# Optimization experiments

Measured on AMD Instinct MI355X. Metric: run time of the kernel, lower is better.

## Reference

```python
import jax, jax.numpy as jnp
import numpy as np

D_MODEL = 1024
NUM_HEADS = 16
HEAD_DIM = D_MODEL // NUM_HEADS
B, T = 4, 2048


def setup_inputs() -> dict:
    key = jax.random.key(0)
    ks = jax.random.split(key, 6)
    s = 1.0 / np.sqrt(D_MODEL)  # ~ nn.Linear init scale
    return {
        "x_q": jax.random.normal(ks[0], (B, T, D_MODEL), jnp.float32),
        "x_kv": jax.random.normal(ks[1], (B, T, D_MODEL), jnp.float32),
        "Wq": jax.random.uniform(ks[2], (D_MODEL, D_MODEL), jnp.float32, -s, s),
        "Wk": jax.random.uniform(ks[3], (D_MODEL, D_MODEL), jnp.float32, -s, s),
        "Wv": jax.random.uniform(ks[4], (D_MODEL, D_MODEL), jnp.float32, -s, s),
        "Wo": jax.random.uniform(ks[5], (D_MODEL, D_MODEL), jnp.float32, -s, s),
    }


def reference(x_q, x_kv, Wq, Wk, Wv, Wo):
    Bq, Tq, C = x_q.shape
    Tk = x_kv.shape[1]
    # torch nn.Linear: y = x @ W.T
    q = (x_q @ Wq.T).reshape(Bq, Tq, NUM_HEADS, HEAD_DIM).transpose(0, 2, 1, 3)
    k = (x_kv @ Wk.T).reshape(Bq, Tk, NUM_HEADS, HEAD_DIM).transpose(0, 2, 1, 3)
    v = (x_kv @ Wv.T).reshape(Bq, Tk, NUM_HEADS, HEAD_DIM).transpose(0, 2, 1, 3)
    scores = jnp.einsum("bhqd,bhkd->bhqk", q, k) / jnp.sqrt(
        jnp.asarray(HEAD_DIM, x_q.dtype)
    )
    causal = jnp.triu(jnp.ones((Tq, Tk), bool), k=1)  # True above diagonal
    scores = jnp.where(causal, -jnp.inf, scores)
    attn = jax.nn.softmax(scores, axis=-1)
    out = jnp.einsum("bhqk,bhkd->bhqd", attn, v)
    out = out.transpose(0, 2, 1, 3).reshape(Bq, Tq, C)
    return out @ Wo.T
```

## Files before the change

kernel.cpp:

```cpp
#include <hip/hip_runtime.h>
#include <stdint.h>

#define T_SEQ 2048
#define NH 16
#define HD 64
#define DM 1024
#define BB 4
#define MROWS (BB * T_SEQ)

typedef __attribute__((ext_vector_type(8))) __bf16 bf16x8;
typedef __attribute__((ext_vector_type(8))) unsigned short u16x8;
typedef __attribute__((ext_vector_type(4))) unsigned short u16x4;
typedef __attribute__((ext_vector_type(4))) float f32x4;

__device__ __forceinline__ unsigned short f2bf(float f) {
  unsigned int x = __float_as_uint(f);
  x = (x + 0x7fffu + ((x >> 16) & 1u)) >> 16;
  return (unsigned short)x;
}

__device__ __forceinline__ bf16x8 ld8_f32(const float* __restrict__ p) {
  f32x4 a = *(const f32x4*)p;
  f32x4 b = *(const f32x4*)(p + 4);
  u16x8 u;
#pragma unroll
  for (int i = 0; i < 4; ++i) {
    u[i]     = f2bf(a[i]);
    u[i + 4] = f2bf(b[i]);
  }
  return __builtin_bit_cast(bf16x8, u);
}

__device__ __forceinline__ bf16x8 ld8_bf(const unsigned short* p) {
  return __builtin_bit_cast(bf16x8, *(const u16x8*)p);
}

__device__ __forceinline__ bf16x8 ld8_lds(const unsigned short* p) {
  u16x4 a = *(const u16x4*)p;
  u16x4 b = *(const u16x4*)(p + 4);
  return __builtin_bit_cast(bf16x8,
      __builtin_shufflevector(a, b, 0, 1, 2, 3, 4, 5, 6, 7));
}

__device__ __forceinline__ u16x4 lo4(u16x8 v) {
  return __builtin_shufflevector(v, v, 0, 1, 2, 3);
}
__device__ __forceinline__ u16x4 hi4(u16x8 v) {
  return __builtin_shufflevector(v, v, 4, 5, 6, 7);
}

__device__ __forceinline__ void gload_lds16(const unsigned short* g,
                                            unsigned short* l) {
  __builtin_amdgcn_global_load_lds(
      (const __attribute__((address_space(1))) unsigned int*)g,
      (__attribute__((address_space(3))) unsigned int*)l, 16, 0, 0);
}

__global__ __launch_bounds__(256) void conv_f32_bf16(
    const float* __restrict__ src, unsigned short* __restrict__ dst, int n8) {
  const int i = blockIdx.x * 256 + threadIdx.x;
  if (i < n8)
    *(u16x8*)(dst + (size_t)i * 8) =
        __builtin_bit_cast(u16x8, ld8_f32(src + (size_t)i * 8));
}

__global__ __launch_bounds__(256) void conv_w4(
    const float* __restrict__ s0, const float* __restrict__ s1,
    const float* __restrict__ s2, const float* __restrict__ s3,
    unsigned short* __restrict__ d012, unsigned short* __restrict__ d3,
    int n8) {
  const int y = blockIdx.y;
  const float* src = (y == 0) ? s0 : (y == 1) ? s1 : (y == 2) ? s2 : s3;
  unsigned short* dst = (y < 3) ? d012 + (size_t)y * DM * DM : d3;
  const int i = blockIdx.x * 256 + threadIdx.x;
  if (i < n8)
    *(u16x8*)(dst + (size_t)i * 8) =
        __builtin_bit_cast(u16x8, ld8_f32(src + (size_t)i * 8));
}

template <int MODE>
__global__ __launch_bounds__(256) void gemm128(
    const unsigned short* __restrict__ A, const unsigned short* __restrict__ B,
    void* __restrict__ Cv, int M, int N, int K) {
  __shared__ __align__(16) unsigned short As[2][128 * 32];
  __shared__ __align__(16) unsigned short Bs[2][128 * 32];

  const int t = threadIdx.x;
  const int lane = t & 63, wave = t >> 6;
  const int m0 = blockIdx.y * 128, n0 = blockIdx.x * 128;

  const int srow = t >> 2;
  const int scol = (t & 3) * 8;
  const unsigned short* ga0 = A + (size_t)(m0 + srow) * K + scol;
  const unsigned short* ga1 = A + (size_t)(m0 + 64 + srow) * K + scol;
  const unsigned short* gb0 = B + (size_t)(n0 + srow) * K + scol;
  const unsigned short* gb1 = B + (size_t)(n0 + 64 + srow) * K + scol;
  const int lo0 = (wave * 16) * 32, lo1 = (64 + wave * 16) * 32;

  const int mw = (wave >> 1) * 64, nw = (wave & 1) * 64;
  const int fr = lane & 15, fq = (lane >> 4) * 8;

  f32x4 acc[4][4];
#pragma unroll
  for (int i = 0; i < 4; ++i)
#pragma unroll
    for (int j = 0; j < 4; ++j) acc[i][j] = (f32x4){0.f, 0.f, 0.f, 0.f};

  for (int k0 = 0; k0 < K; k0 += 64) {
    __syncthreads();
    gload_lds16(ga0 + k0, &As[0][lo0]);
    gload_lds16(ga1 + k0, &As[0][lo1]);
    gload_lds16(gb0 + k0, &Bs[0][lo0]);
    gload_lds16(gb1 + k0, &Bs[0][lo1]);
    gload_lds16(ga0 + k0 + 32, &As[1][lo0]);
    gload_lds16(ga1 + k0 + 32, &As[1][lo1]);
    gload_lds16(gb0 + k0 + 32, &Bs[1][lo0]);
    gload_lds16(gb1 + k0 + 32, &Bs[1][lo1]);
    __syncthreads();

#pragma unroll
    for (int ks = 0; ks < 2; ++ks) {
      bf16x8 af[4], bfr[4];
#pragma unroll
      for (int i = 0; i < 4; ++i)
        af[i] = ld8_bf(&As[ks][(mw + i * 16 + fr) * 32 + fq]);
#pragma unroll
      for (int j = 0; j < 4; ++j)
        bfr[j] = ld8_bf(&Bs[ks][(nw + j * 16 + fr) * 32 + fq]);
#pragma unroll
      for (int i = 0; i < 4; ++i)
#pragma unroll
        for (int j = 0; j < 4; ++j)
          acc[i][j] = __builtin_amdgcn_mfma_f32_16x16x32_bf16(
              af[i], bfr[j], acc[i][j], 0, 0, 0);
    }
  }

  const int orow = (lane >> 4) * 4, ocol = lane & 15;
#pragma unroll
  for (int i = 0; i < 4; ++i)
#pragma unroll
    for (int j = 0; j < 4; ++j) {
      if constexpr (MODE == 2) {
        const int mb = m0 + mw + i * 16 + orow;
        const int n = n0 + nw + j * 16 + ocol;
        u16x4 pk;
#pragma unroll
        for (int r = 0; r < 4; ++r) pk[r] = f2bf(acc[i][j][r]);
        unsigned short* dst = (unsigned short*)Cv +
            ((size_t)((mb >> 11) * NH + (n >> 6)) * HD + (n & 63)) * T_SEQ +
            (mb & 2047);
        *(u16x4*)dst = pk;
      } else {
#pragma unroll
        for (int r = 0; r < 4; ++r) {
          const size_t idx = (size_t)(m0 + mw + i * 16 + orow + r) * N +
                             (n0 + nw + j * 16 + ocol);
          if constexpr (MODE == 1)
            ((float*)Cv)[idx] = acc[i][j][r];
          else
            ((unsigned short*)Cv)[idx] = f2bf(acc[i][j][r]);
        }
      }
    }
}

#define ASTR 68

__global__ __launch_bounds__(256, 2) void attn_flash2(
    const unsigned short* Qw, const unsigned short* __restrict__ Kw,
    const unsigned short* __restrict__ Vt, unsigned short* Ow) {
  __shared__ __align__(16) unsigned short k_lds[2][64][ASTR];
  __shared__ __align__(16) unsigned short vt_lds[2][64][ASTR];
  __shared__ __align__(16) unsigned short p_lds[4][32][ASTR];
  __shared__ float alpha_lds[4][32];
  __shared__ float l_lds[4][32];

  const int tid = threadIdx.x, lane = tid & 63, wave = tid >> 6;
  const int c16 = lane & 15, quad = lane >> 4;
  const int b = blockIdx.z, h = blockIdx.y;
  const int pi = blockIdx.x;
  const int qb0A = (15 - pi) * 128;
  const int qb0B = pi * 128;
  const size_t rkbase = (size_t)b * T_SEQ * DM + (size_t)h * HD;
  const size_t vtbase = (size_t)(b * NH + h) * HD * T_SEQ;

  const int q_loA = qb0A + wave * 32;
  const int q_loB = qb0B + wave * 32;

  bf16x8 qfA[2][2], qfB[2][2];
#pragma unroll
  for (int nf = 0; nf < 2; ++nf) {
    const unsigned short* qpA =
        Qw + rkbase + (size_t)(q_loA + nf * 16 + c16) * DM + quad * 8;
    qfA[nf][0] = ld8_bf(qpA);
    qfA[nf][1] = ld8_bf(qpA + 32);
    const unsigned short* qpB =
        Qw + rkbase + (size_t)(q_loB + nf * 16 + c16) * DM + quad * 8;
    qfB[nf][0] = ld8_bf(qpB);
    qfB[nf][1] = ld8_bf(qpB + 32);
  }

  f32x4 oA[2][4], oB[2][4];
#pragma unroll
  for (int nf = 0; nf < 2; ++nf)
#pragma unroll
    for (int j = 0; j < 4; ++j) {
      oA[nf][j] = (f32x4){0.f, 0.f, 0.f, 0.f};
      oB[nf][j] = (f32x4){0.f, 0.f, 0.f, 0.f};
    }
  float mA[2] = {-3.0e38f, -3.0e38f}, lA[2] = {0.f, 0.f};
  float mB[2] = {-3.0e38f, -3.0e38f}, lB[2] = {0.f, 0.f};

  const int srow = tid >> 2;
  const int scol = (tid & 3) * 16;
  const int ntiles = (qb0A + 191) >> 6;
  const int ntA_w = (q_loA + 95) >> 6;
  const int ntB_w = (q_loB + 95) >> 6;

  const unsigned short* kp0 = Kw + rkbase + (size_t)srow * DM + scol;
  const unsigned short* vp0 = Vt + vtbase + (size_t)srow * T_SEQ + scol;

  auto subtile = [&](const bf16x8 (&qf)[2][2], f32x4 (&o)[2][4],
                     float (&m_r)[2], float (&l_r)[2], const int q_lo,
                     const int kb0, const int bi) {
    f32x4 s[4][2];
    __builtin_amdgcn_s_setprio(1);
#pragma unroll
    for (int mf = 0; mf < 4; ++mf) {
      const unsigned short* kr = &k_lds[bi][mf * 16 + c16][quad * 8];
      const bf16x8 k0 = ld8_lds(kr);
      const bf16x8 k1 = ld8_lds(kr + 32);
#pragma unroll
      for (int nf = 0; nf < 2; ++nf) {
        f32x4 a = {0.f, 0.f, 0.f, 0.f};
        a = __builtin_amdgcn_mfma_f32_16x16x32_bf16(k0, qf[nf][0], a, 0, 0, 0);
        a = __builtin_amdgcn_mfma_f32_16x16x32_bf16(k1, qf[nf][1], a, 0, 0, 0);
        s[mf][nf] = a;
      }
    }
    __builtin_amdgcn_s_setprio(0);
    if (kb0 + 63 > q_lo) {
#pragma unroll
      for (int mf = 0; mf < 4; ++mf) {
        const int key0 = kb0 + mf * 16 + quad * 4;
#pragma unroll
        for (int nf = 0; nf < 2; ++nf) {
          const int qg = q_lo + nf * 16 + c16;
#pragma unroll
          for (int r = 0; r < 4; ++r)
            s[mf][nf][r] =
                (key0 + r <= qg) ? s[mf][nf][r] * 0.125f : -3.0e38f;
        }
      }
    } else {
#pragma unroll
      for (int mf = 0; mf < 4; ++mf)
#pragma unroll
        for (int nf = 0; nf < 2; ++nf)
#pragma unroll
          for (int r = 0; r < 4; ++r) s[mf][nf][r] *= 0.125f;
    }

#pragma unroll
    for (int nf = 0; nf < 2; ++nf) {
      float mx = -3.0e38f;
#pragma unroll
      for (int mf = 0; mf < 4; ++mf)
#pragma unroll
        for (int r = 0; r < 4; ++r) mx = fmaxf(mx, s[mf][nf][r]);
      mx = fmaxf(mx, __shfl_xor(mx, 16, 64));
      mx = fmaxf(mx, __shfl_xor(mx, 32, 64));
      const float m_new = fmaxf(m_r[nf], mx);
      const float al = __expf(m_r[nf] - m_new);
      m_r[nf] = m_new;
      float ps = 0.f;
#pragma unroll
      for (int mf = 0; mf < 4; ++mf) {
        u16x4 pk;
#pragma unroll
        for (int r = 0; r < 4; ++r) {
          const float e = __expf(s[mf][nf][r] - m_new);
          ps += e;
          pk[r] = f2bf(e);
        }
        *(u16x4*)&p_lds[wave][nf * 16 + c16][mf * 16 + quad * 4] = pk;
      }
      ps += __shfl_xor(ps, 16, 64);
      ps += __shfl_xor(ps, 32, 64);
      l_r[nf] = l_r[nf] * al + ps;
      if (quad == 0) alpha_lds[wave][nf * 16 + c16] = al;
    }
    __threadfence_block();

#pragma unroll
    for (int nf = 0; nf < 2; ++nf) {
      float alr[4];
#pragma unroll
      for (int r = 0; r < 4; ++r)
        alr[r] = alpha_lds[wave][nf * 16 + quad * 4 + r];
#pragma unroll
      for (int j = 0; j < 4; ++j)
#pragma unroll
        for (int r = 0; r < 4; ++r) o[nf][j][r] *= alr[r];
    }

    bf16x8 pf[2][2];
#pragma unroll
    for (int nf = 0; nf < 2; ++nf) {
      const unsigned short* pw = &p_lds[wave][nf * 16 + c16][quad * 8];
      pf[nf][0] = ld8_lds(pw);
      pf[nf][1] = ld8_lds(pw + 32);
    }
    __builtin_amdgcn_s_setprio(1);
#pragma unroll
    for (int j = 0; j < 4; ++j) {
      const unsigned short* vr = &vt_lds[bi][j * 16 + c16][quad * 8];
      const bf16x8 v0 = ld8_lds(vr);
      const bf16x8 v1 = ld8_lds(vr + 32);
#pragma unroll
      for (int nf = 0; nf < 2; ++nf) {
        o[nf][j] = __builtin_amdgcn_mfma_f32_16x16x32_bf16(pf[nf][0], v0,
                                                           o[nf][j], 0, 0, 0);
        o[nf][j] = __builtin_amdgcn_mfma_f32_16x16x32_bf16(pf[nf][1], v1,
                                                           o[nf][j], 0, 0, 0);
      }
    }
    __builtin_amdgcn_s_setprio(0);
  };

  {
    u16x8 ka = *(const u16x8*)kp0;
    u16x8 kc = *(const u16x8*)(kp0 + 8);
    u16x8 va = *(const u16x8*)vp0;
    u16x8 vc = *(const u16x8*)(vp0 + 8);
    *(u16x4*)&k_lds[0][srow][scol]       = lo4(ka);
    *(u16x4*)&k_lds[0][srow][scol + 4]   = hi4(ka);
    *(u16x4*)&k_lds[0][srow][scol + 8]   = lo4(kc);
    *(u16x4*)&k_lds[0][srow][scol + 12]  = hi4(kc);
    *(u16x4*)&vt_lds[0][srow][scol]      = lo4(va);
    *(u16x4*)&vt_lds[0][srow][scol + 4]  = hi4(va);
    *(u16x4*)&vt_lds[0][srow][scol + 8]  = lo4(vc);
    *(u16x4*)&vt_lds[0][srow][scol + 12] = hi4(vc);
  }
  __syncthreads();

  int cur = 0;
  for (int t = 0; t < ntiles; ++t) {
    const int kb0 = t * 64;
    const bool pf = (t + 1 < ntiles);
    u16x8 ka, kc, va, vc;
    if (pf) {
      const unsigned short* kp = kp0 + (size_t)(kb0 + 64) * DM;
      ka = *(const u16x8*)kp;
      kc = *(const u16x8*)(kp + 8);
      const unsigned short* vp = vp0 + (kb0 + 64);
      va = *(const u16x8*)vp;
      vc = *(const u16x8*)(vp + 8);
    }
    if (t < ntA_w) subtile(qfA, oA, mA, lA, q_loA, kb0, cur);
    if (t < ntB_w) subtile(qfB, oB, mB, lB, q_loB, kb0, cur);
    if (pf) {
      const int nb = cur ^ 1;
      *(u16x4*)&k_lds[nb][srow][scol]       = lo4(ka);
      *(u16x4*)&k_lds[nb][srow][scol + 4]   = hi4(ka);
      *(u16x4*)&k_lds[nb][srow][scol + 8]   = lo4(kc);
      *(u16x4*)&k_lds[nb][srow][scol + 12]  = hi4(kc);
      *(u16x4*)&vt_lds[nb][srow][scol]      = lo4(va);
      *(u16x4*)&vt_lds[nb][srow][scol + 4]  = hi4(va);
      *(u16x4*)&vt_lds[nb][srow][scol + 8]  = lo4(vc);
      *(u16x4*)&vt_lds[nb][srow][scol + 12] = hi4(vc);
      __syncthreads();
      cur = nb;
    }
  }

  auto epi = [&](f32x4 (&o)[2][4], float (&l_r)[2], const int q_lo) {
    if (quad == 0) {
      l_lds[wave][c16] = l_r[0];
      l_lds[wave][16 + c16] = l_r[1];
    }
    __threadfence_block();
#pragma unroll
    for (int nf = 0; nf < 2; ++nf)
#pragma unroll
      for (int r = 0; r < 4; ++r) {
        const int qg = q_lo + nf * 16 + quad * 4 + r;
        const float inv = 1.0f / l_lds[wave][nf * 16 + quad * 4 + r];
        unsigned short* orow = Ow + rkbase + (size_t)qg * DM;
#pragma unroll
        for (int j = 0; j < 4; ++j)
          orow[j * 16 + c16] = f2bf(o[nf][j][r] * inv);
      }
  };
  epi(oA, lA, q_loA);
  __threadfence_block();
  epi(oB, lB, q_loB);
}

extern "C" void kernel_launch(void* const* d_in, const int* in_sizes, int n_in,
                              void* d_out, int out_size, void* d_ws, size_t ws_size,
                              hipStream_t stream) {
  const float* x_q  = (const float*)d_in[0];
  const float* x_kv = (const float*)d_in[1];
  const float* Wq   = (const float*)d_in[2];
  const float* Wk   = (const float*)d_in[3];
  const float* Wv   = (const float*)d_in[4];
  const float* Wo   = (const float*)d_in[5];
  float* out = (float*)d_out;

  unsigned short* scr  = (unsigned short*)d_out;
  unsigned short* Sx   = scr;
  unsigned short* Wk_b = scr + (size_t)MROWS * DM;
  unsigned short* Wv_b = Wk_b + (size_t)DM * DM;
  unsigned short* Wq_b = Wv_b + (size_t)DM * DM;

  unsigned short* qb   = (unsigned short*)d_ws;
  unsigned short* kb   = qb + (size_t)MROWS * DM;
  unsigned short* vtb  = kb + (size_t)MROWS * DM;
  unsigned short* Wo_b = vtb + (size_t)MROWS * DM;

  const int nW8 = DM * DM / 8;
  const int nX8 = MROWS * DM / 8;

  conv_w4<<<dim3(nW8 / 256, 4), 256, 0, stream>>>(Wk, Wv, Wq, Wo, Wk_b, Wo_b,
                                                  nW8);
  conv_f32_bf16<<<nX8 / 256, 256, 0, stream>>>(x_kv, Sx, nX8);

  dim3 gg(DM / 128, MROWS / 128);
  gemm128<0><<<gg, 256, 0, stream>>>(Sx, Wk_b, kb, MROWS, DM, DM);
  gemm128<2><<<gg, 256, 0, stream>>>(Sx, Wv_b, vtb, MROWS, DM, DM);
  conv_f32_bf16<<<nX8 / 256, 256, 0, stream>>>(x_q, Sx, nX8);
  gemm128<0><<<gg, 256, 0, stream>>>(Sx, Wq_b, qb, MROWS, DM, DM);
  attn_flash2<<<dim3(8, NH, BB), 256, 0, stream>>>(qb, kb, vtb, qb);
  gemm128<1><<<gg, 256, 0, stream>>>(qb, Wo_b, out, MROWS, DM, DM);
}
```

Before: 317.4 us.

## Interleave A/B query subtiles in attention, swizzle GEMM blocks by XCD, use native bf16 cvt

The attention loop now handles both query subtiles (A and B) in one fused body. Each K and V fragment is read from LDS once and fed to the MFMAs of both subtiles, and each subtile gets its own P and alpha buffers. The GEMM remaps block indices so consecutive blocks on the same XCD share M rows, aiming for better L2 reuse. The float-to-bf16 rounding is replaced with the native __bf16 conversion. Holding two sets of S and P fragments at once raises register pressure, and the per-subtile buffers add LDS use, which may hurt occupancy at launch_bounds(256,2).

```diff
diff --git a/kernel.cpp b/kernel.cpp
--- a/kernel.cpp
+++ b/kernel.cpp
@@ -14,9 +14,7 @@
 typedef __attribute__((ext_vector_type(4))) float f32x4;
 
 __device__ __forceinline__ unsigned short f2bf(float f) {
-  unsigned int x = __float_as_uint(f);
-  x = (x + 0x7fffu + ((x >> 16) & 1u)) >> 16;
-  return (unsigned short)x;
+  return __builtin_bit_cast(unsigned short, (__bf16)f);
 }
 
 __device__ __forceinline__ bf16x8 ld8_f32(const float* __restrict__ p) {
@@ -87,7 +85,10 @@
 
   const int t = threadIdx.x;
   const int lane = t & 63, wave = t >> 6;
-  const int m0 = blockIdx.y * 128, n0 = blockIdx.x * 128;
+  const int lin = (int)(blockIdx.x + gridDim.x * blockIdx.y);
+  const int xcd = lin & 7, slot = lin >> 3;
+  const int m0 = (xcd * 8 + (slot >> 3)) * 128;
+  const int n0 = (slot & 7) * 128;
 
   const int srow = t >> 2;
   const int scol = (t & 3) * 8;
@@ -172,8 +173,10 @@
     const unsigned short* __restrict__ Vt, unsigned short* Ow) {
   __shared__ __align__(16) unsigned short k_lds[2][64][ASTR];
   __shared__ __align__(16) unsigned short vt_lds[2][64][ASTR];
-  __shared__ __align__(16) unsigned short p_lds[4][32][ASTR];
-  __shared__ float alpha_lds[4][32];
+  __shared__ __align__(16) unsigned short pA_lds[4][32][ASTR];
+  __shared__ __align__(16) unsigned short pB_lds[4][32][ASTR];
+  __shared__ float alA_lds[4][32];
+  __shared__ float alB_lds[4][32];
   __shared__ float l_lds[4][32];
 
   const int tid = threadIdx.x, lane = tid & 63, wave = tid >> 6;
@@ -221,25 +224,9 @@
   const unsigned short* kp0 = Kw + rkbase + (size_t)srow * DM + scol;
   const unsigned short* vp0 = Vt + vtbase + (size_t)srow * T_SEQ + scol;
 
-  auto subtile = [&](const bf16x8 (&qf)[2][2], f32x4 (&o)[2][4],
-                     float (&m_r)[2], float (&l_r)[2], const int q_lo,
-                     const int kb0, const int bi) {
-    f32x4 s[4][2];
-    __builtin_amdgcn_s_setprio(1);
-#pragma unroll
-    for (int mf = 0; mf < 4; ++mf) {
-      const unsigned short* kr = &k_lds[bi][mf * 16 + c16][quad * 8];
-      const bf16x8 k0 = ld8_lds(kr);
-      const bf16x8 k1 = ld8_lds(kr + 32);
-#pragma unroll
-      for (int nf = 0; nf < 2; ++nf) {
-        f32x4 a = {0.f, 0.f, 0.f, 0.f};
-        a = __builtin_amdgcn_mfma_f32_16x16x32_bf16(k0, qf[nf][0], a, 0, 0, 0);
-        a = __builtin_amdgcn_mfma_f32_16x16x32_bf16(k1, qf[nf][1], a, 0, 0, 0);
-        s[mf][nf] = a;
-      }
-    }
-    __builtin_amdgcn_s_setprio(0);
+  auto mask_sm = [&](f32x4 (&s)[4][2], float* m_r, float* l_r, const int q_lo,
+                     const int kb0, unsigned short (*pl)[ASTR],
+                     float* al_row) {
     if (kb0 + 63 > q_lo) {
 #pragma unroll
       for (int mf = 0; mf < 4; ++mf) {
@@ -261,7 +248,6 @@
 #pragma unroll
           for (int r = 0; r < 4; ++r) s[mf][nf][r] *= 0.125f;
     }
-
 #pragma unroll
     for (int nf = 0; nf < 2; ++nf) {
       float mx = -3.0e38f;
@@ -284,49 +270,27 @@
           ps += e;
           pk[r] = f2bf(e);
         }
-        *(u16x4*)&p_lds[wave][nf * 16 + c16][mf * 16 + quad * 4] = pk;
+        *(u16x4*)&pl[nf * 16 + c16][mf * 16 + quad * 4] = pk;
       }
       ps += __shfl_xor(ps, 16, 64);
       ps += __shfl_xor(ps, 32, 64);
       l_r[nf] = l_r[nf] * al + ps;
-      if (quad == 0) alpha_lds[wave][nf * 16 + c16] = al;
-    }
-    __threadfence_block();
-
+      if (quad == 0) al_row[nf * 16 + c16] = al;
+    }
+  };
+
+  auto rescale = [&](f32x4 (&o)[2][4], const float* al_row) {
 #pragma unroll
     for (int nf = 0; nf < 2; ++nf) {
       float alr[4];
 #pragma unroll
       for (int r = 0; r < 4; ++r)
-        alr[r] = alpha_lds[wave][nf * 16 + quad * 4 + r];
+        alr[r] = al_row[nf * 16 + quad * 4 + r];
 #pragma unroll
       for (int j = 0; j < 4; ++j)
 #pragma unroll
         for (int r = 0; r < 4; ++r) o[nf][j][r] *= alr[r];
     }
-
-    bf16x8 pf[2][2];
-#pragma unroll
-    for (int nf = 0; nf < 2; ++nf) {
-      const unsigned short* pw = &p_lds[wave][nf * 16 + c16][quad * 8];
-      pf[nf][0] = ld8_lds(pw);
-      pf[nf][1] = ld8_lds(pw + 32);
-    }
-    __builtin_amdgcn_s_setprio(1);
-#pragma unroll
-    for (int j = 0; j < 4; ++j) {
-      const unsigned short* vr = &vt_lds[bi][j * 16 + c16][quad * 8];
-      const bf16x8 v0 = ld8_lds(vr);
-      const bf16x8 v1 = ld8_lds(vr + 32);
-#pragma unroll
-      for (int nf = 0; nf < 2; ++nf) {
-        o[nf][j] = __builtin_amdgcn_mfma_f32_16x16x32_bf16(pf[nf][0], v0,
-                                                           o[nf][j], 0, 0, 0);
-        o[nf][j] = __builtin_amdgcn_mfma_f32_16x16x32_bf16(pf[nf][1], v1,
-                                                           o[nf][j], 0, 0, 0);
-      }
-    }
-    __builtin_amdgcn_s_setprio(0);
   };
 
   {
@@ -358,8 +322,83 @@
       va = *(const u16x8*)vp;
       vc = *(const u16x8*)(vp + 8);
     }
-    if (t < ntA_w) subtile(qfA, oA, mA, lA, q_loA, kb0, cur);
-    if (t < ntB_w) subtile(qfB, oB, mB, lB, q_loB, kb0, cur);
+
+    if (t < ntA_w) {
+      const bool doB = (t < ntB_w);
+      f32x4 sA[4][2], sB[4][2];
+      __builtin_amdgcn_s_setprio(1);
+#pragma unroll
+      for (int mf = 0; mf < 4; ++mf) {
+        const unsigned short* kr = &k_lds[cur][mf * 16 + c16][quad * 8];
+        const bf16x8 k0 = ld8_lds(kr);
+        const bf16x8 k1 = ld8_lds(kr + 32);
+#pragma unroll
+        for (int nf = 0; nf < 2; ++nf) {
+          f32x4 a = {0.f, 0.f, 0.f, 0.f};
+          a = __builtin_amdgcn_mfma_f32_16x16x32_bf16(k0, qfA[nf][0], a, 0, 0, 0);
+          a = __builtin_amdgcn_mfma_f32_16x16x32_bf16(k1, qfA[nf][1], a, 0, 0, 0);
+          sA[mf][nf] = a;
+        }
+        if (doB) {
+#pragma unroll
+          for (int nf = 0; nf < 2; ++nf) {
+            f32x4 a = {0.f, 0.f, 0.f, 0.f};
+            a = __builtin_amdgcn_mfma_f32_16x16x32_bf16(k0, qfB[nf][0], a, 0, 0, 0);
+            a = __builtin_amdgcn_mfma_f32_16x16x32_bf16(k1, qfB[nf][1], a, 0, 0, 0);
+            sB[mf][nf] = a;
+          }
+        }
+      }
+      __builtin_amdgcn_s_setprio(0);
+
+      mask_sm(sA, mA, lA, q_loA, kb0, pA_lds[wave], alA_lds[wave]);
+      if (doB) mask_sm(sB, mB, lB, q_loB, kb0, pB_lds[wave], alB_lds[wave]);
+      __threadfence_block();
+
+      rescale(oA, alA_lds[wave]);
+      if (doB) rescale(oB, alB_lds[wave]);
+
+      bf16x8 pfA[2][2], pfB[2][2];
+#pragma unroll
+      for (int nf = 0; nf < 2; ++nf) {
+        const unsigned short* pw = &pA_lds[wave][nf * 16 + c16][quad * 8];
+        pfA[nf][0] = ld8_lds(pw);
+        pfA[nf][1] = ld8_lds(pw + 32);
+      }
+      if (doB) {
+#pragma unroll
+        for (int nf = 0; nf < 2; ++nf) {
+          const unsigned short* pw = &pB_lds[wave][nf * 16 + c16][quad * 8];
+          pfB[nf][0] = ld8_lds(pw);
+          pfB[nf][1] = ld8_lds(pw + 32);
+        }
+      }
+      __builtin_amdgcn_s_setprio(1);
+#pragma unroll
+      for (int j = 0; j < 4; ++j) {
+        const unsigned short* vr = &vt_lds[cur][j * 16 + c16][quad * 8];
+        const bf16x8 v0 = ld8_lds(vr);
+        const bf16x8 v1 = ld8_lds(vr + 32);
+#pragma unroll
+        for (int nf = 0; nf < 2; ++nf) {
+          oA[nf][j] = __builtin_amdgcn_mfma_f32_16x16x32_bf16(pfA[nf][0], v0,
+                                                              oA[nf][j], 0, 0, 0);
+          oA[nf][j] = __builtin_amdgcn_mfma_f32_16x16x32_bf16(pfA[nf][1], v1,
+                                                              oA[nf][j], 0, 0, 0);
+        }
+        if (doB) {
+#pragma unroll
+          for (int nf = 0; nf < 2; ++nf) {
+            oB[nf][j] = __builtin_amdgcn_mfma_f32_16x16x32_bf16(
+                pfB[nf][0], v0, oB[nf][j], 0, 0, 0);
+            oB[nf][j] = __builtin_amdgcn_mfma_f32_16x16x32_bf16(
+                pfB[nf][1], v1, oB[nf][j], 0, 0, 0);
+          }
+        }
+      }
+      __builtin_amdgcn_s_setprio(0);
+    }
+
     if (pf) {
       const int nb = cur ^ 1;
       *(u16x4*)&k_lds[nb][srow][scol]       = lo4(ka);
```

After: 327.0 us. 1.03x slower.

## Fuse K and V projections into one GEMM and remap blocks per XCD

Applied to the files above, without the earlier changes.

Merges the K and V projection GEMMs into a single launch with N=2048, using the contiguous Wk/Wv bf16 buffers, and routes each output tile to either row-major K or transposed V. Adds a block-index remap so each group of blocks on one XCD covers a contiguous range of M rows, aiming for better L2 reuse of A tiles. Also swaps the manual bf16 rounding for the compiler's native float-to-bf16 conversion. Together these cut one launch and one re-read of the activations, at the cost of a bigger grid and a remap that assumes the row-tile count divides by 8.

```diff
diff --git a/kernel.cpp b/kernel.cpp
--- a/kernel.cpp
+++ b/kernel.cpp
@@ -14,9 +14,7 @@
 typedef __attribute__((ext_vector_type(4))) float f32x4;
 
 __device__ __forceinline__ unsigned short f2bf(float f) {
-  unsigned int x = __float_as_uint(f);
-  x = (x + 0x7fffu + ((x >> 16) & 1u)) >> 16;
-  return (unsigned short)x;
+  return __builtin_bit_cast(unsigned short, (__bf16)f);
 }
 
 __device__ __forceinline__ bf16x8 ld8_f32(const float* __restrict__ p) {
@@ -81,13 +79,18 @@
 template <int MODE>
 __global__ __launch_bounds__(256) void gemm128(
     const unsigned short* __restrict__ A, const unsigned short* __restrict__ B,
-    void* __restrict__ Cv, int M, int N, int K) {
+    void* __restrict__ Cv, void* __restrict__ Cv2, int M, int N, int K) {
   __shared__ __align__(16) unsigned short As[2][128 * 32];
   __shared__ __align__(16) unsigned short Bs[2][128 * 32];
 
   const int t = threadIdx.x;
   const int lane = t & 63, wave = t >> 6;
-  const int m0 = blockIdx.y * 128, n0 = blockIdx.x * 128;
+  const int lin = (int)(blockIdx.x + gridDim.x * blockIdx.y);
+  const int nx = N >> 7;
+  const int mpx = (M >> 7) >> 3;
+  const int xcd = lin & 7, slot = lin >> 3;
+  const int m0 = (xcd * mpx + slot / nx) * 128;
+  const int n0 = (slot % nx) * 128;
 
   const int srow = t >> 2;
   const int scol = (t & 3) * 8;
@@ -137,6 +140,7 @@
   }
 
   const int orow = (lane >> 4) * 4, ocol = lane & 15;
+  const bool kv_lo = (MODE == 3) && (n0 < DM);
 #pragma unroll
   for (int i = 0; i < 4; ++i)
 #pragma unroll
@@ -151,6 +155,25 @@
             ((size_t)((mb >> 11) * NH + (n >> 6)) * HD + (n & 63)) * T_SEQ +
             (mb & 2047);
         *(u16x4*)dst = pk;
+      } else if constexpr (MODE == 3) {
+        const int mb = m0 + mw + i * 16 + orow;
+        const int n = n0 + nw + j * 16 + ocol;
+        if (kv_lo) {
+#pragma unroll
+          for (int r = 0; r < 4; ++r)
+            ((unsigned short*)Cv)[(size_t)(mb + r) * DM + n] =
+                f2bf(acc[i][j][r]);
+        } else {
+          const int nv = n - DM;
+          u16x4 pk;
+#pragma unroll
+          for (int r = 0; r < 4; ++r) pk[r] = f2bf(acc[i][j][r]);
+          unsigned short* dst = (unsigned short*)Cv2 +
+              ((size_t)((mb >> 11) * NH + (nv >> 6)) * HD + (nv & 63)) *
+                  T_SEQ +
+              (mb & 2047);
+          *(u16x4*)dst = pk;
+        }
       } else {
 #pragma unroll
         for (int r = 0; r < 4; ++r) {
@@ -427,11 +450,12 @@
                                                   nW8);
   conv_f32_bf16<<<nX8 / 256, 256, 0, stream>>>(x_kv, Sx, nX8);
 
-  dim3 gg(DM / 128, MROWS / 128);
-  gemm128<0><<<gg, 256, 0, stream>>>(Sx, Wk_b, kb, MROWS, DM, DM);
-  gemm128<2><<<gg, 256, 0, stream>>>(Sx, Wv_b, vtb, MROWS, DM, DM);
+  gemm128<3><<<dim3(2 * DM / 128, MROWS / 128), 256, 0, stream>>>(
+      Sx, Wk_b, kb, vtb, MROWS, 2 * DM, DM);
   conv_f32_bf16<<<nX8 / 256, 256, 0, stream>>>(x_q, Sx, nX8);
-  gemm128<0><<<gg, 256, 0, stream>>>(Sx, Wq_b, qb, MROWS, DM, DM);
+  gemm128<0><<<dim3(DM / 128, MROWS / 128), 256, 0, stream>>>(
+      Sx, Wq_b, qb, nullptr, MROWS, DM, DM);
   attn_flash2<<<dim3(8, NH, BB), 256, 0, stream>>>(qb, kb, vtb, qb);
-  gemm128<1><<<gg, 256, 0, stream>>>(qb, Wo_b, out, MROWS, DM, DM);
-}
+  gemm128<1><<<dim3(DM / 128, MROWS / 128), 256, 0, stream>>>(
+      qb, Wo_b, out, nullptr, MROWS, DM, DM);
+}
```

Result: faster. 302.9 us (-4.5%).
